# Performance work log

Measured on AMD Instinct MI355X. Metric: run time of the kernel, lower is better.

## Reference

```python
import jax, jax.numpy as jnp
import numpy as np

KEY_DIM = 32
NUM_HEADS = 8
ATTN_RATIO = 2
D = ATTN_RATIO * KEY_DIM          # 64, per-head value dim
DH = D * NUM_HEADS                # 512
NH_KD = KEY_DIM * NUM_HEADS       # 256
H_QKV = DH + 2 * NH_KD            # 1024
DIM = 512
IMG = 1024                        # img_shape (32x32)
S = 32                            # sqrt(IMG)
ATT = 1044                        # att_shape = N
B = 16
EPS = 1e-5


def hardswish(x):
    return x * jnp.clip(x + 3.0, 0.0, 6.0) / 6.0


def setup_inputs() -> dict:
    key = jax.random.key(0)
    ks = jax.random.split(key, 8)
    x = jax.random.normal(ks[0], (B, ATT, DIM), dtype=jnp.float32)
    qkv_w = jax.random.normal(ks[1], (H_QKV, DIM), dtype=jnp.float32) * 0.02
    bn_gamma = jnp.ones((H_QKV,), dtype=jnp.float32)
    bn_beta = jnp.zeros((H_QKV,), dtype=jnp.float32)
    bn_mean = jax.random.normal(ks[2], (H_QKV,), dtype=jnp.float32) * 0.01
    bn_var = jax.random.uniform(ks[3], (H_QKV,), minval=0.5, maxval=1.5, dtype=jnp.float32)
    conv_w = jax.random.normal(ks[4], (DH, 1, 3, 3), dtype=jnp.float32) * 0.1  # depthwise
    conv_b = jnp.zeros((DH,), dtype=jnp.float32)
    proj_w = jax.random.normal(ks[5], (IMG, ATT), dtype=jnp.float32) * 0.02
    proj_b = jnp.zeros((IMG,), dtype=jnp.float32)
    out_w = jax.random.normal(ks[6], (DIM, DH), dtype=jnp.float32) * 0.02
    out_b = jnp.zeros((DIM,), dtype=jnp.float32)
    return {"x": x, "qkv_w": qkv_w, "bn_gamma": bn_gamma, "bn_beta": bn_beta,
            "bn_mean": bn_mean, "bn_var": bn_var, "conv_w": conv_w, "conv_b": conv_b,
            "proj_w": proj_w, "proj_b": proj_b, "out_w": out_w, "out_b": out_b}


def reference(x, qkv_w, bn_gamma, bn_beta, bn_mean, bn_var,
              conv_w, conv_b, proj_w, proj_b, out_w, out_b):
    Bb, N, C = x.shape
    # Linear_BN: linear (no bias) + BatchNorm1d (eval, running stats)
    qkv = jnp.einsum('bnc,hc->bnh', x, qkv_w)
    qkv = (qkv - bn_mean) * (bn_gamma * jax.lax.rsqrt(bn_var + EPS)) + bn_beta
    qkv = qkv.reshape(Bb, N, NUM_HEADS, 2 * KEY_DIM + D)
    q = qkv[..., :KEY_DIM].transpose(0, 2, 1, 3)                 # (B,H,N,kd)
    k = qkv[..., KEY_DIM:2 * KEY_DIM].transpose(0, 2, 1, 3)      # (B,H,N,kd)
    v = qkv[..., 2 * KEY_DIM:].transpose(0, 2, 1, 3)             # (B,H,N,d)
    # parallel depthwise conv branch: raw reshape (B,H,IMG,d) -> (B,DH,S,S), as in torch
    v0 = v[:, :, :IMG, :].reshape(Bb, DH, S, S)
    vc = jax.lax.conv_general_dilated(
        hardswish(v0), conv_w, window_strides=(1, 1), padding='SAME',
        dimension_numbers=('NCHW', 'OIHW', 'NCHW'), feature_group_count=DH)
    vc = (vc + conv_b[None, :, None, None]).reshape(Bb, DH, IMG)  # (B,DH,IMG)
    # attention
    attn = jax.nn.softmax(jnp.einsum('bhnk,bhmk->bhnm', q, k) * (KEY_DIM ** -0.5), axis=-1)
    o = jnp.einsum('bhnm,bhmd->bhnd', attn, v)                   # (B,H,N,d)
    # torch: (attn@v).transpose(1,2).reshape(B,-1,N) -> raw flatten of (B,N,H,d) into (B,DH,N)
    o = o.transpose(0, 2, 1, 3).reshape(Bb, DH, N)
    xo = jnp.einsum('bdn,mn->bdm', o, proj_w) + proj_b + vc       # (B,DH,IMG)
    out = jnp.einsum('bmd,cd->bmc', xo.transpose(0, 2, 1), out_w) + out_b  # (B,IMG,DIM)
    return out
```

## Files before the change

### kernel.cpp

```cpp
#include <hip/hip_runtime.h>
#include <hip/hip_fp16.h>

typedef _Float16 f16;
typedef _Float16 f16x8 __attribute__((ext_vector_type(8)));
typedef _Float16 f16x4 __attribute__((ext_vector_type(4)));
typedef float    f32x4 __attribute__((ext_vector_type(4)));
typedef float    f32x16 __attribute__((ext_vector_type(16)));

#define DEV __device__ __forceinline__

DEV int imin(int a, int b) { return a < b ? a : b; }

#if defined(__has_builtin)
#  if __has_builtin(__builtin_amdgcn_exp2f)
#    define EXP2(x) __builtin_amdgcn_exp2f(x)
#  else
#    define EXP2(x) __expf((x) * 0.6931471805599453f)
#  endif
#else
#  define EXP2(x) __expf((x) * 0.6931471805599453f)
#endif

#define QSCALE (0.17677669529663687f * 1.4426950408889634f)


constexpr size_t OFF_XH   = 0;
constexpr size_t OFF_WQ   = 17104896;
constexpr size_t OFF_PW   = 18153472;
constexpr size_t OFF_OW   = 20316160;
constexpr size_t OFF_BNA  = 20840448;
constexpr size_t OFF_BNB  = 20844544;
constexpr size_t OFF_QB   = 20848640;
constexpr size_t OFF_KB   = 30285824;
constexpr size_t OFF_VT   = 39198720;
constexpr size_t OFF_OPAD = 57024512;
constexpr size_t OFF_VCT  = 74326016;
constexpr size_t OFF_XOT  = 91103232;

DEV f32x16 zero16() {
  f32x16 z;
  #pragma unroll
  for (int i = 0; i < 16; ++i) z[i] = 0.f;
  return z;
}

DEV unsigned pk2(float a, float b) {
  auto h = __builtin_amdgcn_cvt_pkrtz(a, b);
  union { decltype(h) x; unsigned u; } t;
  t.x = h;
  return t.u;
}

DEV void plswap(unsigned &a, unsigned &b) {
  asm("v_permlane32_swap_b32 %0, %1" : "+v"(a), "+v"(b));
}

union W4 { unsigned w[4]; f16x8 v; };

DEV void pack_block(const float p[16], f16x8 &a0, f16x8 &a1) {
  unsigned w0 = pk2(p[0], p[1]),   w1 = pk2(p[2], p[3]);
  unsigned w2 = pk2(p[4], p[5]),   w3 = pk2(p[6], p[7]);
  unsigned w4 = pk2(p[8], p[9]),   w5 = pk2(p[10], p[11]);
  unsigned w6 = pk2(p[12], p[13]), w7 = pk2(p[14], p[15]);
  plswap(w0, w2); plswap(w1, w3);
  plswap(w4, w6); plswap(w5, w7);
  W4 u; u.w[0] = w0; u.w[1] = w1; u.w[2] = w2; u.w[3] = w3; a0 = u.v;
  W4 v; v.w[0] = w4; v.w[1] = w5; v.w[2] = w6; v.w[3] = w7; a1 = v.v;
}

__global__ __launch_bounds__(256) void prep_kernel(
    const float* __restrict__ x, const float* __restrict__ qkv_w,
    const float* __restrict__ bn_g, const float* __restrict__ bn_b,
    const float* __restrict__ bn_m, const float* __restrict__ bn_v,
    const float* __restrict__ proj_w, const float* __restrict__ out_w,
    f16* __restrict__ x_h, f16* __restrict__ wq_h, f16* __restrict__ pw_h,
    f16* __restrict__ ow_h, float* __restrict__ bn_a, float* __restrict__ bn_sh,
    f16* __restrict__ qb, f16* __restrict__ kb, f16* __restrict__ vt,
    f16* __restrict__ opad)
{
  long tid = (long)blockIdx.x * blockDim.x + threadIdx.x;
  long gsz = (long)gridDim.x * blockDim.x;

  for (long i = tid; i < 2138112; i += gsz) {
    float4 f = ((const float4*)x)[i];
    f16x4 o = {(f16)f.x, (f16)f.y, (f16)f.z, (f16)f.w};
    ((f16x4*)x_h)[i] = o;
  }
  for (long i = tid; i < 524288; i += gsz) wq_h[i] = (f16)qkv_w[i];
  for (long i = tid; i < 1081344; i += gsz) {
    long m = i / 1056, nn = i - m * 1056;
    pw_h[i] = (nn < 1044) ? (f16)proj_w[m * 1044 + nn] : (f16)0.f;
  }
  for (long i = tid; i < 262144; i += gsz) ow_h[i] = (f16)out_w[i];
  for (long i = tid; i < 1024; i += gsz) {
    float a = bn_g[i] * rsqrtf(bn_v[i] + 1e-5f);
    bn_a[i] = a;
    bn_sh[i] = bn_b[i] - bn_m[i] * a;
  }
  for (long i = tid; i < 13824; i += gsz) {
    int bh = (int)(i / 108);
    int nn = 1044 + (int)(i - (long)bh * 108);
    f16* q = qb + ((long)bh * 1152 + nn) * 32;
    for (int j = 0; j < 32; ++j) q[j] = (f16)0.f;
  }
  for (long i = tid; i < 5632; i += gsz) {
    int bh = (int)(i / 44);
    int nn = 1044 + (int)(i - (long)bh * 44);
    f16* k = kb + ((long)bh * 1088 + nn) * 32;
    for (int j = 0; j < 32; ++j) k[j] = (f16)0.f;
  }
  for (long i = tid; i < 8192; i += gsz) {
    f16* v = vt + i * 1088 + 1044;
    for (int j = 0; j < 44; ++j) v[j] = (f16)0.f;
  }
  for (long i = tid; i < 8192; i += gsz) {
    f16* o = opad + i * 1056 + 1044;
    for (int j = 0; j < 12; ++j) o[j] = (f16)0.f;
  }
}

DEV void gemm_core(const f16* __restrict__ A, const f16* __restrict__ B,
                   int lda, int ldb, int kIters, int rowClampA, int rowClampB,
                   f16* As, f16* Bs, f32x4 acc[4][4])
{
  const int t = threadIdx.x;
  const int wave = t >> 6, lane = t & 63;
  const int wr = wave >> 1, wc = wave & 1;
  const int r0 = t >> 2, seg = t & 3;
  const int fr = lane & 15, fg = lane >> 4;
  const int ra0 = imin(r0, rowClampA);
  const int ra1 = imin(r0 + 64, rowClampA);
  const int rb0 = imin(r0, rowClampB);
  const int rb1 = imin(r0 + 64, rowClampB);

  const f16* pa0 = A + (long)ra0 * lda + seg * 8;
  const f16* pa1 = A + (long)ra1 * lda + seg * 8;
  const f16* pb0 = B + (long)rb0 * ldb + seg * 8;
  const f16* pb1 = B + (long)rb1 * ldb + seg * 8;

  f16x8 a0, a1, b0, b1;
  a0 = *(const f16x8*)(pa0);
  a1 = *(const f16x8*)(pa1);
  b0 = *(const f16x8*)(pb0);
  b1 = *(const f16x8*)(pb1);

  #pragma unroll 1
  for (int kt = 0; kt < kIters; ++kt) {
    __syncthreads();
    *(f16x8*)(As + r0 * 40 + seg * 8) = a0;
    *(f16x8*)(As + (r0 + 64) * 40 + seg * 8) = a1;
    *(f16x8*)(Bs + r0 * 40 + seg * 8) = b0;
    *(f16x8*)(Bs + (r0 + 64) * 40 + seg * 8) = b1;
    __syncthreads();
    if (kt + 1 < kIters) {
      const int kb = (kt + 1) * 32;
      a0 = *(const f16x8*)(pa0 + kb);
      a1 = *(const f16x8*)(pa1 + kb);
      b0 = *(const f16x8*)(pb0 + kb);
      b1 = *(const f16x8*)(pb1 + kb);
    }
    f16x8 af[4], bf[4];
    #pragma unroll
    for (int m = 0; m < 4; ++m)
      af[m] = *(const f16x8*)(As + (wr * 64 + m * 16 + fr) * 40 + fg * 8);
    #pragma unroll
    for (int n = 0; n < 4; ++n)
      bf[n] = *(const f16x8*)(Bs + (wc * 64 + n * 16 + fr) * 40 + fg * 8);
    #pragma unroll
    for (int m = 0; m < 4; ++m)
      #pragma unroll
      for (int n = 0; n < 4; ++n)
        acc[m][n] = __builtin_amdgcn_mfma_f32_16x16x32_f16(af[m], bf[n], acc[m][n], 0, 0, 0);
  }
}

__global__ __launch_bounds__(256) void qkv_gemm(
    const f16* __restrict__ x_h, const f16* __restrict__ wq,
    const float* __restrict__ bn_a, const float* __restrict__ bn_sh,
    f16* __restrict__ qb, f16* __restrict__ kb, f16* __restrict__ vt)
{
  __shared__ f16 As[128 * 40];
  __shared__ f16 Bs[128 * 40];
  const int id = blockIdx.x + blockIdx.y * 8;
  const int lin = (id & 7) * 131 + (id >> 3);
  const int row0 = (lin & 7) * 128;
  const int col0 = (lin >> 3) * 128;
  f32x4 acc[4][4];
  #pragma unroll
  for (int m = 0; m < 4; ++m)
    #pragma unroll
    for (int n = 0; n < 4; ++n) acc[m][n] = (f32x4){0.f, 0.f, 0.f, 0.f};
  gemm_core(wq + (long)row0 * 512, x_h + (long)col0 * 512, 512, 512, 16,
            1 << 30, 16703 - col0, As, Bs, acc);
  const int lane = threadIdx.x & 63, wave = threadIdx.x >> 6;
  const int wr = wave >> 1, wc = wave & 1, fr = lane & 15, fg = lane >> 4;
  #pragma unroll
  for (int m = 0; m < 4; ++m) {
    const int chBase = row0 + wr * 64 + m * 16 + fg * 4;
    const float4 ba4 = *(const float4*)(bn_a + chBase);
    const float4 bs4 = *(const float4*)(bn_sh + chBase);
    const int hh = chBase >> 7, r = chBase & 127;
    #pragma unroll
    for (int n = 0; n < 4; ++n) {
      int tok = col0 + wc * 64 + n * 16 + fr;
      if (tok < 16704) {
        int bi = tok / 1044;
        int ni = tok - bi * 1044;
        long bh = (long)(bi * 8 + hh);
        float v0 = acc[m][n][0] * ba4.x + bs4.x;
        float v1 = acc[m][n][1] * ba4.y + bs4.y;
        float v2 = acc[m][n][2] * ba4.z + bs4.z;
        float v3 = acc[m][n][3] * ba4.w + bs4.w;
        if (r < 32) {
          f16x4 pk = {(f16)(v0 * QSCALE), (f16)(v1 * QSCALE),
                      (f16)(v2 * QSCALE), (f16)(v3 * QSCALE)};
          *(f16x4*)(qb + (bh * 1152 + ni) * 32 + r) = pk;
        } else if (r < 64) {
          f16x4 pk = {(f16)v0, (f16)v1, (f16)v2, (f16)v3};
          *(f16x4*)(kb + (bh * 1088 + ni) * 32 + (r - 32)) = pk;
        } else {
          f16* vp = vt + (bh * 64 + (r - 64)) * 1088 + ni;
          vp[0]        = (f16)v0;
          vp[1088]     = (f16)v1;
          vp[2 * 1088] = (f16)v2;
          vp[3 * 1088] = (f16)v3;
        }
      }
    }
  }
}

__global__ __launch_bounds__(256) void conv_kernel(
    const f16* __restrict__ vt, const float* __restrict__ conv_w,
    const float* __restrict__ conv_b, f16* __restrict__ vcT)
{
  __shared__ f16 img[16][34][36];
  const int b = blockIdx.y, g = blockIdx.x;
  const int c0 = g * 16, h = c0 >> 6, ci0 = c0 & 63;
  const int t = threadIdx.x;
  for (int i = t; i < 16 * 34 * 36; i += 256) ((f16*)img)[i] = (f16)0.f;
  __syncthreads();
  const int d = t >> 2, seg = t & 3;
  const f16* src = vt + ((long)(b * 8 + h) * 64 + d) * 1088 + ci0 * 16 + seg * 64;
  const int dhib = d >> 5;
  const int s2 = d & 31;
  #pragma unroll
  for (int j = 0; j < 8; ++j) {
    f16x8 vv = *(const f16x8*)(src + j * 8);
    #pragma unroll
    for (int e = 0; e < 8; ++e) {
      int local = seg * 64 + j * 8 + e;
      int cl = local >> 4, rr = local & 15;
      float xv = (float)vv[e];
      float hs = xv * fminf(fmaxf(xv + 3.f, 0.f), 6.f) * (1.f / 6.f);
      img[cl][1 + rr * 2 + dhib][1 + s2] = (f16)hs;
    }
  }
  __syncthreads();
  const int cl = t & 15, pg = t >> 4;
  const int c = c0 + cl;
  float w[9];
  #pragma unroll
  for (int i = 0; i < 9; ++i) w[i] = conv_w[c * 9 + i];
  const float bias = conv_b[c];
  for (int i = 0; i < 64; ++i) {
    int p = pg + i * 16;
    int s1 = p >> 5, ss2 = p & 31;
    float a = bias;
    #pragma unroll
    for (int di = 0; di < 3; ++di)
      #pragma unroll
      for (int dj = 0; dj < 3; ++dj)
        a += w[di * 3 + dj] * (float)img[cl][s1 + di][ss2 + dj];
    vcT[((long)b * 1024 + p) * 512 + c] = (f16)a;
  }
}

__global__ __launch_bounds__(256) void attn_kernel(
    const f16* __restrict__ qb, const f16* __restrict__ kb,
    const f16* __restrict__ vt, f16* __restrict__ opad)
{
  __shared__ f16 kls[2][4 * 64 * 8];
  __shared__ f16 vls[2][8 * 64 * 8];
  __shared__ float l_sh[4][32];

  const int id = blockIdx.x + blockIdx.y * 9;
  const int xcd = id & 7, sl = id >> 3;
  const int bh = xcd * 16 + sl / 9, qblk = sl % 9;
  const int b = bh >> 3, h = bh & 7;
  const int t = threadIdx.x;
  const int wave = t >> 6, lane = t & 63;
  const int lq = lane & 31, hi = lane >> 5;
  const int q0 = qblk * 128 + wave * 32;

  const f16* qb_ = qb + (long)bh * 1152 * 32;
  const f16* kb_ = kb + (long)bh * 1088 * 32;
  const f16* vt_ = vt + (long)bh * 64 * 1088;

  const f16x8 qf0 = *(const f16x8*)(qb_ + (long)(q0 + lq) * 32 + hi * 8);
  const f16x8 qf1 = *(const f16x8*)(qb_ + (long)(q0 + lq) * 32 + 16 + hi * 8);

  const int sk_k = t >> 2, sk_s = t & 3;
  const int sv_d = t >> 3, sv_p = t & 7;
  const int wkoff  = (sk_s * 64 + ((sk_k + sk_s) & 63)) * 16;
  const int wvoff0 = (sv_p * 64 + ((sv_d + sv_p) & 63)) * 16;
  const int wvoff1 = (sv_p * 64 + ((sv_d + 32 + sv_p) & 63)) * 16;
  int koff[2][2], voff[2][4];
  #pragma unroll
  for (int blk = 0; blk < 2; ++blk)
    #pragma unroll
    for (int ss = 0; ss < 2; ++ss) {
      int ss2 = 2 * ss + hi;
      koff[blk][ss] = (ss2 * 64 + ((blk * 32 + lq + ss2) & 63)) * 16;
    }
  #pragma unroll
  for (int nd = 0; nd < 2; ++nd)
    #pragma unroll
    for (int ks = 0; ks < 4; ++ks) {
      int kk8 = 2 * ks + hi;
      voff[nd][ks] = (kk8 * 64 + ((nd * 32 + lq + kk8) & 63)) * 16;
    }

  f16x8 stk, stv0, stv1;
  auto load_tile = [&](int kt) {
    stk  = *(const f16x8*)(kb_ + (long)(kt * 64 + sk_k) * 32 + sk_s * 8);
    stv0 = *(const f16x8*)(vt_ + (long)sv_d * 1088 + kt * 64 + sv_p * 8);
    stv1 = *(const f16x8*)(vt_ + (long)(sv_d + 32) * 1088 + kt * 64 + sv_p * 8);
  };
  auto write_tile = [&](int buf) {
    *(f16x8*)((char*)kls[buf] + wkoff)  = stk;
    *(f16x8*)((char*)vls[buf] + wvoff0) = stv0;
    *(f16x8*)((char*)vls[buf] + wvoff1) = stv1;
  };

  f32x16 o0 = zero16(), o1 = zero16();
  float lsum = 0.f;

  load_tile(0);
  write_tile(0);
  __syncthreads();

  int cur = 0;
  #pragma unroll 1
  for (int kt = 0; kt < 17; ++kt) {
    if (kt < 16) load_tile(kt + 1);
    const char* kcur = (const char*)kls[cur];
    const char* vcur = (const char*)vls[cur];
    f16x8 kf[2][2];
    #pragma unroll
    for (int blk = 0; blk < 2; ++blk)
      #pragma unroll
      for (int ss = 0; ss < 2; ++ss)
        kf[blk][ss] = *(const f16x8*)(kcur + koff[blk][ss]);
    f32x16 s0 = zero16(), s1 = zero16();
    s0 = __builtin_amdgcn_mfma_f32_32x32x16_f16(kf[0][0], qf0, s0, 0, 0, 0);
    s0 = __builtin_amdgcn_mfma_f32_32x32x16_f16(kf[0][1], qf1, s0, 0, 0, 0);
    s1 = __builtin_amdgcn_mfma_f32_32x32x16_f16(kf[1][0], qf0, s1, 0, 0, 0);
    s1 = __builtin_amdgcn_mfma_f32_32x32x16_f16(kf[1][1], qf1, s1, 0, 0, 0);
    float p0[16], p1[16];
    #pragma unroll
    for (int r = 0; r < 16; ++r) { p0[r] = EXP2(s0[r]); p1[r] = EXP2(s1[r]); }
    if (kt == 16) {
      #pragma unroll
      for (int r = 0; r < 16; ++r) {
        int cr = (r & 3) + 8 * (r >> 2) + 4 * hi;
        p0[r] = (cr < 20) ? p0[r] : 0.f;
        p1[r] = 0.f;
      }
    }
    float t8[8];
    #pragma unroll
    for (int r = 0; r < 8; ++r) t8[r] = (p0[r] + p0[r + 8]) + (p1[r] + p1[r + 8]);
    lsum += ((t8[0] + t8[1]) + (t8[2] + t8[3])) + ((t8[4] + t8[5]) + (t8[6] + t8[7]));
    f16x8 pa[4];
    pack_block(p0, pa[0], pa[1]);
    pack_block(p1, pa[2], pa[3]);
    #pragma unroll
    for (int ks = 0; ks < 4; ++ks) {
      f16x8 vf0 = *(const f16x8*)(vcur + voff[0][ks]);
      f16x8 vf1 = *(const f16x8*)(vcur + voff[1][ks]);
      o0 = __builtin_amdgcn_mfma_f32_32x32x16_f16(pa[ks], vf0, o0, 0, 0, 0);
      o1 = __builtin_amdgcn_mfma_f32_32x32x16_f16(pa[ks], vf1, o1, 0, 0, 0);
    }
    if (kt < 16) write_tile(cur ^ 1);
    __syncthreads();
    cur ^= 1;
  }

  lsum += __shfl_xor(lsum, 32);
  l_sh[wave][lq] = lsum;
  __syncthreads();
  float invl[16];
  #pragma unroll
  for (int r = 0; r < 16; ++r) {
    int cr = (r & 3) + 8 * (r >> 2) + 4 * hi;
    invl[r] = __builtin_amdgcn_rcpf(l_sh[wave][cr]);
  }
  #pragma unroll
  for (int nd = 0; nd < 2; ++nd) {
    #pragma unroll
    for (int r = 0; r < 16; ++r) {
      int cr = (r & 3) + 8 * (r >> 2) + 4 * hi;
      int q = q0 + cr;
      if (q < 1044) {
        float val = (nd ? o1[r] : o0[r]) * invl[r];
        unsigned flat = (unsigned)q * 512u + (unsigned)h * 64u + (unsigned)(nd * 32 + lq);
        unsigned c = flat / 1044u;
        unsigned np = flat - c * 1044u;
        opad[((long)b * 512 + c) * 1056 + np] = (f16)val;
      }
    }
  }
}

__global__ __launch_bounds__(256) void proj_gemm(
    const f16* __restrict__ pw, const f16* __restrict__ opad,
    const float* __restrict__ proj_b, const f16* __restrict__ vcT,
    f16* __restrict__ xoT)
{
  __shared__ f16 As[128 * 40];
  __shared__ f16 Bs[128 * 40];
  const int id = blockIdx.x + blockIdx.y * 4 + blockIdx.z * 32;
  const int lin = (id & 7) * 64 + (id >> 3);
  const int b = lin >> 5;
  const int rc = lin & 31;
  const int row0 = (rc >> 2) * 128;
  const int col0 = (rc & 3) * 128;
  f32x4 acc[4][4];
  #pragma unroll
  for (int m = 0; m < 4; ++m)
    #pragma unroll
    for (int n = 0; n < 4; ++n) acc[m][n] = (f32x4){0.f, 0.f, 0.f, 0.f};
  gemm_core(pw + (long)row0 * 1056, opad + ((long)b * 512 + col0) * 1056,
            1056, 1056, 33, 1 << 30, 1 << 30, As, Bs, acc);
  const int lane = threadIdx.x & 63, wave = threadIdx.x >> 6;
  const int wr = wave >> 1, wc = wave & 1, fr = lane & 15, fg = lane >> 4;
  #pragma unroll
  for (int m = 0; m < 4; ++m) {
    #pragma unroll
    for (int rr = 0; rr < 4; ++rr) {
      int mi = row0 + wr * 64 + m * 16 + fg * 4 + rr;
      float pb = proj_b[mi];
      #pragma unroll
      for (int n = 0; n < 4; ++n) {
        int c = col0 + wc * 64 + n * 16 + fr;
        long idx = ((long)b * 1024 + mi) * 512 + c;
        xoT[idx] = (f16)(acc[m][n][rr] + pb + (float)vcT[idx]);
      }
    }
  }
}

__global__ __launch_bounds__(256) void out_gemm(
    const f16* __restrict__ xoT, const f16* __restrict__ ow,
    const float* __restrict__ out_b, float* __restrict__ out)
{
  __shared__ f16 As[128 * 40];
  __shared__ f16 Bs[128 * 40];
  const int id = blockIdx.x + blockIdx.y * 4 + blockIdx.z * 32;
  const int lin = (id & 7) * 64 + (id >> 3);
  const int b = lin >> 5;
  const int rc = lin & 31;
  const int row0 = (rc >> 2) * 128;
  const int col0 = (rc & 3) * 128;
  f32x4 acc[4][4];
  #pragma unroll
  for (int m = 0; m < 4; ++m)
    #pragma unroll
    for (int n = 0; n < 4; ++n) acc[m][n] = (f32x4){0.f, 0.f, 0.f, 0.f};
  gemm_core(xoT + ((long)b * 1024 + row0) * 512, ow + (long)col0 * 512,
            512, 512, 16, 1 << 30, 1 << 30, As, Bs, acc);
  const int lane = threadIdx.x & 63, wave = threadIdx.x >> 6;
  const int wr = wave >> 1, wc = wave & 1, fr = lane & 15, fg = lane >> 4;
  float ob[4];
  #pragma unroll
  for (int n = 0; n < 4; ++n) ob[n] = out_b[col0 + wc * 64 + n * 16 + fr];
  #pragma unroll
  for (int m = 0; m < 4; ++m) {
    #pragma unroll
    for (int rr = 0; rr < 4; ++rr) {
      int mi = row0 + wr * 64 + m * 16 + fg * 4 + rr;
      #pragma unroll
      for (int n = 0; n < 4; ++n) {
        int co = col0 + wc * 64 + n * 16 + fr;
        out[((long)b * 1024 + mi) * 512 + co] = acc[m][n][rr] + ob[n];
      }
    }
  }
}

extern "C" void kernel_launch(void* const* d_in, const int* in_sizes, int n_in,
                              void* d_out, int out_size, void* d_ws, size_t ws_size,
                              hipStream_t stream) {
  const float* x      = (const float*)d_in[0];
  const float* qkv_w  = (const float*)d_in[1];
  const float* bn_g   = (const float*)d_in[2];
  const float* bn_b   = (const float*)d_in[3];
  const float* bn_m   = (const float*)d_in[4];
  const float* bn_v   = (const float*)d_in[5];
  const float* conv_w = (const float*)d_in[6];
  const float* conv_b = (const float*)d_in[7];
  const float* proj_w = (const float*)d_in[8];
  const float* proj_b = (const float*)d_in[9];
  const float* out_w  = (const float*)d_in[10];
  const float* out_b  = (const float*)d_in[11];
  float* out = (float*)d_out;

  char* ws = (char*)d_ws;
  f16*   x_h   = (f16*)(ws + OFF_XH);
  f16*   wq_h  = (f16*)(ws + OFF_WQ);
  f16*   pw_h  = (f16*)(ws + OFF_PW);
  f16*   ow_h  = (f16*)(ws + OFF_OW);
  float* bn_a  = (float*)(ws + OFF_BNA);
  float* bn_sh = (float*)(ws + OFF_BNB);
  f16*   qb    = (f16*)(ws + OFF_QB);
  f16*   kb    = (f16*)(ws + OFF_KB);
  f16*   vt    = (f16*)(ws + OFF_VT);
  f16*   opad  = (f16*)(ws + OFF_OPAD);
  f16*   vcT   = (f16*)(ws + OFF_VCT);
  f16*   xoT   = (f16*)(ws + OFF_XOT);

  prep_kernel<<<1024, 256, 0, stream>>>(x, qkv_w, bn_g, bn_b, bn_m, bn_v,
                                        proj_w, out_w, x_h, wq_h, pw_h, ow_h,
                                        bn_a, bn_sh, qb, kb, vt, opad);
  qkv_gemm<<<dim3(8, 131), 256, 0, stream>>>(x_h, wq_h, bn_a, bn_sh, qb, kb, vt);
  conv_kernel<<<dim3(32, 16), 256, 0, stream>>>(vt, conv_w, conv_b, vcT);
  attn_kernel<<<dim3(9, 128), 256, 0, stream>>>(qb, kb, vt, opad);
  proj_gemm<<<dim3(4, 8, 16), 256, 0, stream>>>(pw_h, opad, proj_b, vcT, xoT);
  out_gemm<<<dim3(4, 8, 16), 256, 0, stream>>>(xoT, ow_h, out_b, out);
}
```

Baseline: 175.3 us.

## Halve attention key tile to 32 and raise occupancy with launch bounds

The attention kernel now processes 32 keys per iteration instead of 64, using one score accumulator instead of two. This halves LDS buffers and live registers, and the launch bound requests 4 blocks per CU for more occupancy. It also raises MFMA wave priority around the PV matmul. The cost is twice as many loop iterations and __syncthreads barriers, with smaller global loads per tile.

```diff
diff --git a/kernel.cpp b/kernel.cpp
--- a/kernel.cpp
+++ b/kernel.cpp
@@ -276,12 +276,12 @@
   }
 }
 
-__global__ __launch_bounds__(256) void attn_kernel(
+__global__ __launch_bounds__(256, 4) void attn_kernel(
     const f16* __restrict__ qb, const f16* __restrict__ kb,
     const f16* __restrict__ vt, f16* __restrict__ opad)
 {
-  __shared__ f16 kls[2][4 * 64 * 8];
-  __shared__ f16 vls[2][8 * 64 * 8];
+  __shared__ f16 kls[2][4 * 32 * 8];
+  __shared__ f16 vls[2][4 * 64 * 8];
   __shared__ float l_sh[4][32];
 
   const int id = blockIdx.x + blockIdx.y * 9;
@@ -300,37 +300,34 @@
   const f16x8 qf0 = *(const f16x8*)(qb_ + (long)(q0 + lq) * 32 + hi * 8);
   const f16x8 qf1 = *(const f16x8*)(qb_ + (long)(q0 + lq) * 32 + 16 + hi * 8);
 
-  const int sk_k = t >> 2, sk_s = t & 3;
-  const int sv_d = t >> 3, sv_p = t & 7;
-  const int wkoff  = (sk_s * 64 + ((sk_k + sk_s) & 63)) * 16;
-  const int wvoff0 = (sv_p * 64 + ((sv_d + sv_p) & 63)) * 16;
-  const int wvoff1 = (sv_p * 64 + ((sv_d + 32 + sv_p) & 63)) * 16;
-  int koff[2][2], voff[2][4];
-  #pragma unroll
-  for (int blk = 0; blk < 2; ++blk)
-    #pragma unroll
-    for (int ss = 0; ss < 2; ++ss) {
-      int ss2 = 2 * ss + hi;
-      koff[blk][ss] = (ss2 * 64 + ((blk * 32 + lq + ss2) & 63)) * 16;
-    }
+  const int sk_k = t >> 3, sk_s8 = t & 7;
+  const int sk_seg = sk_s8 >> 1, sk_half = sk_s8 & 1;
+  const int sv_d = t >> 2, sv_p = t & 3;
+  const int wkoff = (sk_seg * 32 + ((sk_k + sk_seg) & 31)) * 16 + sk_half * 8;
+  const int wvoff = (sv_p * 64 + ((sv_d + sv_p) & 63)) * 16;
+  int koff[2], voff[2][2];
+  #pragma unroll
+  for (int ss = 0; ss < 2; ++ss) {
+    int ss2 = 2 * ss + hi;
+    koff[ss] = (ss2 * 32 + ((lq + ss2) & 31)) * 16;
+  }
   #pragma unroll
   for (int nd = 0; nd < 2; ++nd)
     #pragma unroll
-    for (int ks = 0; ks < 4; ++ks) {
-      int kk8 = 2 * ks + hi;
-      voff[nd][ks] = (kk8 * 64 + ((nd * 32 + lq + kk8) & 63)) * 16;
-    }
-
-  f16x8 stk, stv0, stv1;
+    for (int ks = 0; ks < 2; ++ks) {
+      int kk4 = 2 * ks + hi;
+      voff[nd][ks] = (kk4 * 64 + ((nd * 32 + lq + kk4) & 63)) * 16;
+    }
+
+  f16x4 stk;
+  f16x8 stv;
   auto load_tile = [&](int kt) {
-    stk  = *(const f16x8*)(kb_ + (long)(kt * 64 + sk_k) * 32 + sk_s * 8);
-    stv0 = *(const f16x8*)(vt_ + (long)sv_d * 1088 + kt * 64 + sv_p * 8);
-    stv1 = *(const f16x8*)(vt_ + (long)(sv_d + 32) * 1088 + kt * 64 + sv_p * 8);
+    stk = *(const f16x4*)(kb_ + (long)(kt * 32 + sk_k) * 32 + sk_s8 * 4);
+    stv = *(const f16x8*)(vt_ + (long)sv_d * 1088 + kt * 32 + sv_p * 8);
   };
   auto write_tile = [&](int buf) {
-    *(f16x8*)((char*)kls[buf] + wkoff)  = stk;
-    *(f16x8*)((char*)vls[buf] + wvoff0) = stv0;
-    *(f16x8*)((char*)vls[buf] + wvoff1) = stv1;
+    *(f16x4*)((char*)kls[buf] + wkoff) = stk;
+    *(f16x8*)((char*)vls[buf] + wvoff) = stv;
   };
 
   f32x16 o0 = zero16(), o1 = zero16();
@@ -342,47 +339,44 @@
 
   int cur = 0;
   #pragma unroll 1
-  for (int kt = 0; kt < 17; ++kt) {
-    if (kt < 16) load_tile(kt + 1);
+  for (int kt = 0; kt < 33; ++kt) {
+    if (kt < 32) load_tile(kt + 1);
     const char* kcur = (const char*)kls[cur];
     const char* vcur = (const char*)vls[cur];
-    f16x8 kf[2][2];
-    #pragma unroll
-    for (int blk = 0; blk < 2; ++blk)
-      #pragma unroll
-      for (int ss = 0; ss < 2; ++ss)
-        kf[blk][ss] = *(const f16x8*)(kcur + koff[blk][ss]);
-    f32x16 s0 = zero16(), s1 = zero16();
-    s0 = __builtin_amdgcn_mfma_f32_32x32x16_f16(kf[0][0], qf0, s0, 0, 0, 0);
-    s0 = __builtin_amdgcn_mfma_f32_32x32x16_f16(kf[0][1], qf1, s0, 0, 0, 0);
-    s1 = __builtin_amdgcn_mfma_f32_32x32x16_f16(kf[1][0], qf0, s1, 0, 0, 0);
-    s1 = __builtin_amdgcn_mfma_f32_32x32x16_f16(kf[1][1], qf1, s1, 0, 0, 0);
-    float p0[16], p1[16];
-    #pragma unroll
-    for (int r = 0; r < 16; ++r) { p0[r] = EXP2(s0[r]); p1[r] = EXP2(s1[r]); }
-    if (kt == 16) {
+    f16x8 kf0 = *(const f16x8*)(kcur + koff[0]);
+    f16x8 kf1 = *(const f16x8*)(kcur + koff[1]);
+    f32x16 s = zero16();
+    s = __builtin_amdgcn_mfma_f32_32x32x16_f16(kf0, qf0, s, 0, 0, 0);
+    s = __builtin_amdgcn_mfma_f32_32x32x16_f16(kf1, qf1, s, 0, 0, 0);
+    float p[16];
+    #pragma unroll
+    for (int r = 0; r < 16; ++r) p[r] = EXP2(s[r]);
+    if (kt == 32) {
       #pragma unroll
       for (int r = 0; r < 16; ++r) {
         int cr = (r & 3) + 8 * (r >> 2) + 4 * hi;
-        p0[r] = (cr < 20) ? p0[r] : 0.f;
-        p1[r] = 0.f;
+        p[r] = (cr < 20) ? p[r] : 0.f;
       }
     }
     float t8[8];
     #pragma unroll
-    for (int r = 0; r < 8; ++r) t8[r] = (p0[r] + p0[r + 8]) + (p1[r] + p1[r + 8]);
+    for (int r = 0; r < 8; ++r) t8[r] = p[r] + p[r + 8];
     lsum += ((t8[0] + t8[1]) + (t8[2] + t8[3])) + ((t8[4] + t8[5]) + (t8[6] + t8[7]));
-    f16x8 pa[4];
-    pack_block(p0, pa[0], pa[1]);
-    pack_block(p1, pa[2], pa[3]);
-    #pragma unroll
-    for (int ks = 0; ks < 4; ++ks) {
-      f16x8 vf0 = *(const f16x8*)(vcur + voff[0][ks]);
-      f16x8 vf1 = *(const f16x8*)(vcur + voff[1][ks]);
-      o0 = __builtin_amdgcn_mfma_f32_32x32x16_f16(pa[ks], vf0, o0, 0, 0, 0);
-      o1 = __builtin_amdgcn_mfma_f32_32x32x16_f16(pa[ks], vf1, o1, 0, 0, 0);
-    }
-    if (kt < 16) write_tile(cur ^ 1);
+    f16x8 pa0, pa1;
+    pack_block(p, pa0, pa1);
+    __builtin_amdgcn_s_setprio(1);
+    {
+      f16x8 vf00 = *(const f16x8*)(vcur + voff[0][0]);
+      f16x8 vf10 = *(const f16x8*)(vcur + voff[1][0]);
+      o0 = __builtin_amdgcn_mfma_f32_32x32x16_f16(pa0, vf00, o0, 0, 0, 0);
+      o1 = __builtin_amdgcn_mfma_f32_32x32x16_f16(pa0, vf10, o1, 0, 0, 0);
+      f16x8 vf01 = *(const f16x8*)(vcur + voff[0][1]);
+      f16x8 vf11 = *(const f16x8*)(vcur + voff[1][1]);
+      o0 = __builtin_amdgcn_mfma_f32_32x32x16_f16(pa1, vf01, o0, 0, 0, 0);
+      o1 = __builtin_amdgcn_mfma_f32_32x32x16_f16(pa1, vf11, o1, 0, 0, 0);
+    }
+    __builtin_amdgcn_s_setprio(0);
+    if (kt < 32) write_tile(cur ^ 1);
     __syncthreads();
     cur ^= 1;
   }
```

Result: no change. 176.0 us (+0.4%).
